# Kernel tuning notes

Hardware: AMD Instinct MI355X
Metric: run time of the kernel (lower is better)

The kernel has to match this reference:

```python
import jax, jax.numpy as jnp
import numpy as np

CAP = 15.0
EPS = 1e-6
NUM_HEADS = 16
HEAD_DIM = 64

def _rmsnorm(x, w):
    xf = x.astype(jnp.float32)
    var = jnp.mean(xf * xf, axis=-1, keepdims=True)
    return w * (xf * jax.lax.rsqrt(var + EPS)).astype(x.dtype)

def _gate(g):
    # sigmoid(soft_cap(g)) with cap 15
    return jax.nn.sigmoid(CAP * jnp.tanh(g / CAP))

def setup_inputs() -> dict:
    key = jax.random.key(0)
    ks = jax.random.split(key, 4)
    B, S, D = 4, 2048, 1024
    H, Dh = NUM_HEADS, HEAD_DIM
    return {
        "x": jax.random.normal(ks[0], (B, S, D), jnp.float32),
        "hidden_state": jnp.zeros((B, H, Dh, Dh), jnp.float32),
        "w_rms": jnp.ones((D,), jnp.float32),
        "w_qkv": jax.random.normal(ks[1], (D, 3 * H * Dh), jnp.float32) * 0.02,
        "w_gate": jax.random.normal(ks[2], (D, 3 * H), jnp.float32) * 0.02,
        "w_out": jax.random.normal(ks[3], (D, D), jnp.float32) * 0.02,
    }

def reference(x, hidden_state, w_rms, w_qkv, w_gate, w_out):
    B, S, D = x.shape
    H, Dh = NUM_HEADS, HEAD_DIM
    residual = x
    xn = _rmsnorm(x, w_rms)
    qkv = (xn @ w_qkv).reshape(B, S, 3, H, Dh)
    q, k, v = qkv[:, :, 0], qkv[:, :, 1], qkv[:, :, 2]  # [B,S,H,Dh]
    gates = _gate((xn @ w_gate).reshape(B, S, 3, H))
    i_g, f_g, o_g = gates[:, :, 0], gates[:, :, 1], gates[:, :, 2]  # [B,S,H]

    # time-major for scan: [S,B,H,...]
    def tm(a):
        return jnp.moveaxis(a, 1, 0)

    def step(state, inp):
        qt, kt, vt, it, ft, ot = inp  # [B,H,Dh]/[B,H]
        kv = kt[..., :, None] * vt[..., None, :]            # [B,H,Dh,Dh]
        state = ft[..., None, None] * state + it[..., None, None] * kv
        h = jnp.einsum('bhd,bhde->bhe', qt, state) * ot[..., None]
        return state, h

    _, h_seq = jax.lax.scan(step, hidden_state,
                            (tm(q), tm(k), tm(v), tm(i_g), tm(f_g), tm(o_g)))
    out = jnp.moveaxis(h_seq, 0, 1).reshape(B, S, H * Dh) @ w_out
    return residual + out
```

## Files before the change

kernel.cpp:

```cpp
#include <hip/hip_runtime.h>
#include <math.h>

typedef unsigned short u16;
typedef unsigned int   u32;
typedef __bf16 bf16x8 __attribute__((ext_vector_type(8)));
typedef float  f32x4  __attribute__((ext_vector_type(4)));

#define NBATCH 4
#define SEQ    2048
#define DIM    1024
#define NH     16
#define BH     64
#define NC     32
#define ROWS   8192
#define N1     3328

__device__ __forceinline__ u16 f2bf(float f) {
  u32 u = __builtin_bit_cast(u32, f);
  u32 r = u + 0x7fffu + ((u >> 16) & 1u);
  return (u16)(r >> 16);
}
__device__ __forceinline__ float bf2f(u16 h) {
  return __builtin_bit_cast(float, (u32)h << 16);
}

__device__ __forceinline__ void gl2lds16(const u16* g, u16* l) {
  __builtin_amdgcn_global_load_lds(
      (const __attribute__((address_space(1))) u32*)g,
      (__attribute__((address_space(3))) u32*)l, 16, 0, 0);
}

__global__ __launch_bounds__(256) void prep_all(const float* __restrict__ x,
                                                const float* __restrict__ w_rms,
                                                u16* __restrict__ xn,
                                                const float* __restrict__ Wqkv,
                                                const float* __restrict__ Wout,
                                                const float* __restrict__ wg,
                                                u16* __restrict__ BtQkv, u16* __restrict__ BtOut) {
  __shared__ float tile[32][33];
  __shared__ float red[4];
  const int bid = blockIdx.x;
  if (bid < 8192) {
    const int row = bid, tid = threadIdx.x;
    const float4 xv = *(const float4*)&x[(size_t)row * 1024 + tid * 4];
    float ss = xv.x * xv.x + xv.y * xv.y + xv.z * xv.z + xv.w * xv.w;
    #pragma unroll
    for (int off = 32; off > 0; off >>= 1) ss += __shfl_down(ss, off);
    if ((tid & 63) == 0) red[tid >> 6] = ss;
    __syncthreads();
    const float tot = red[0] + red[1] + red[2] + red[3];
    const float scale = rsqrtf(tot * (1.0f / 1024.0f) + 1e-6f);
    const float4 wv = *(const float4*)&w_rms[tid * 4];
    const u16 o0 = f2bf(xv.x * scale * wv.x), o1 = f2bf(xv.y * scale * wv.y);
    const u16 o2 = f2bf(xv.z * scale * wv.z), o3 = f2bf(xv.w * scale * wv.w);
    uint2 ov;
    ov.x = (u32)o0 | ((u32)o1 << 16);
    ov.y = (u32)o2 | ((u32)o3 << 16);
    *(uint2*)&xn[(size_t)row * 1024 + tid * 4] = ov;
  } else {
    const int pb = bid - 8192;
    const int bx = pb % 129, by = pb / 129;
    const int tx = threadIdx.x & 31, ty = threadIdx.x >> 5;
    if (bx < 128) {
      const float* W; u16* Bt; int N, n0;
      if (bx < 96) { W = Wqkv; Bt = BtQkv; N = 3072; n0 = bx * 32; }
      else         { W = Wout; Bt = BtOut; N = 1024; n0 = (bx - 96) * 32; }
      const int k0 = by * 32;
      #pragma unroll
      for (int i = 0; i < 4; i++)
        tile[ty + i * 8][tx] = W[(size_t)(k0 + ty + i * 8) * N + n0 + tx];
      __syncthreads();
      #pragma unroll
      for (int i = 0; i < 4; i++)
        Bt[(size_t)(n0 + ty + i * 8) * 1024 + k0 + tx] = f2bf(tile[tx][ty + i * 8]);
    } else {
      const int tid = threadIdx.x;
      #pragma unroll
      for (int gg = 0; gg < 8; gg++) {
        const int g = by * 8 + gg;
        #pragma unroll
        for (int kk = 0; kk < 4; kk++) {
          const int k = kk * 256 + tid;
          u16 v = 0;
          if (g < 48) v = f2bf(wg[(size_t)k * 48 + g]);
          BtQkv[(size_t)(3072 + g) * 1024 + k] = v;
        }
      }
    }
  }
}


#define FENCE asm volatile("" ::: "memory")
#define SBAR  do { FENCE; __builtin_amdgcn_s_barrier(); FENCE; } while (0)
#define WAITV4 do { FENCE; asm volatile("s_waitcnt vmcnt(4)" ::: "memory"); } while (0)
#define WAITV2 do { FENCE; asm volatile("s_waitcnt vmcnt(2)" ::: "memory"); } while (0)
#define WAITV0 do { FENCE; asm volatile("s_waitcnt vmcnt(0)" ::: "memory"); } while (0)

#define STAGE_A(BUF, HALF, TILE) do { \
  const u16* s_ = Abase + (size_t)(TILE) * 64 + (size_t)(HALF) * 131072; \
  u16* l_ = &lds[((BUF) * 4 + (HALF)) * 8192 + tid * 8]; \
  gl2lds16(s_, l_); gl2lds16(s_ + 65536, l_ + 4096); \
} while (0)

#define STAGE_B(BUF, HALF, TILE) do { \
  const u16* s_ = Bbase + (size_t)(TILE) * 64 + (size_t)(HALF) * 131072; \
  u16* l_ = &lds[((BUF) * 4 + 2 + (HALF)) * 8192 + tid * 8]; \
  gl2lds16(s_, l_); gl2lds16(s_ + 65536, l_ + 4096); \
} while (0)

#define READ_A(ALDS, MH) do { \
  _Pragma("unroll") \
  for (int mi_ = 0; mi_ < 4; ++mi_) { \
    af[mi_][0] = *(const bf16x8*)((ALDS) + (MH) * 4096 + mi_ * 1024 + co0); \
    af[mi_][1] = *(const bf16x8*)((ALDS) + (MH) * 4096 + mi_ * 1024 + co1); \
  } \
} while (0)

#define READ_B(BLDS, NH) do { \
  _Pragma("unroll") \
  for (int ni_ = 0; ni_ < 2; ++ni_) { \
    bfr[NH][ni_][0] = *(const bf16x8*)((BLDS) + (NH) * 2048 + ni_ * 1024 + co0); \
    bfr[NH][ni_][1] = *(const bf16x8*)((BLDS) + (NH) * 2048 + ni_ * 1024 + co1); \
  } \
} while (0)

#define MFMA16(MH, NH) do { \
  __builtin_amdgcn_s_setprio(1); \
  _Pragma("unroll") \
  for (int mi_ = 0; mi_ < 4; ++mi_) { \
    _Pragma("unroll") \
    for (int ni_ = 0; ni_ < 2; ++ni_) { \
      acc[(MH)*4+mi_][(NH)*2+ni_] = __builtin_amdgcn_mfma_f32_16x16x32_bf16( \
          af[mi_][0], bfr[NH][ni_][0], acc[(MH)*4+mi_][(NH)*2+ni_], 0, 0, 0); \
      acc[(MH)*4+mi_][(NH)*2+ni_] = __builtin_amdgcn_mfma_f32_16x16x32_bf16( \
          af[mi_][1], bfr[NH][ni_][1], acc[(MH)*4+mi_][(NH)*2+ni_], 0, 0, 0); \
    } \
  } \
  __builtin_amdgcn_s_setprio(0); \
} while (0)

#define GITER4(T, FULL) do { \
   \
  STAGE_A(1, 0, 2*(T)+1); STAGE_A(1, 1, 2*(T)+1); \
  READ_A(aLds0, 0); READ_B(bLds0, 0); READ_B(bLds0, 1); \
  SBAR; MFMA16(0, 0); MFMA16(0, 1); SBAR; \
   \
  if (FULL) { STAGE_B(0, 0, 2*(T)+2); STAGE_B(0, 1, 2*(T)+2); } \
  READ_A(aLds0, 1); \
  SBAR; MFMA16(1, 0); MFMA16(1, 1); if (FULL) { WAITV4; } else { WAITV0; } SBAR; \
   \
  if (FULL) { STAGE_A(0, 0, 2*(T)+2); STAGE_A(0, 1, 2*(T)+2); } \
  READ_A(aLds1, 0); READ_B(bLds1, 0); READ_B(bLds1, 1); \
  SBAR; MFMA16(0, 0); MFMA16(0, 1); SBAR; \
   \
  if (FULL) { STAGE_B(1, 0, 2*(T)+3); STAGE_B(1, 1, 2*(T)+3); } \
  READ_A(aLds1, 1); \
  SBAR; MFMA16(1, 0); MFMA16(1, 1); if (FULL) { WAITV4; } SBAR; \
} while (0)

#define CORE_SETUP(AROWBASE, BCOLBASE) \
  const int tid = threadIdx.x; \
  const int lane = tid & 63, wave = tid >> 6; \
  const int q = lane >> 4, m16 = lane & 15; \
  const int wm = wave & 1, wn = wave >> 1; \
  const int sx = m16 & 7; \
  const int co0 = (q ^ sx) * 8; \
  const int co1 = ((4 + q) ^ sx) * 8; \
  const int r0 = tid >> 3, pc = tid & 7; \
  const int lcg = pc ^ (r0 & 7); \
  const u16* Abase = (AROWBASE) + (size_t)r0 * 1024 + lcg * 8; \
  const u16* Bbase = (BCOLBASE) + (size_t)r0 * 1024 + lcg * 8; \
  const u16* aLds0 = &lds[wm * 8192 + m16 * 64]; \
  const u16* aLds1 = aLds0 + 32768; \
  const u16* bLds0 = &lds[16384 + (wn >> 1) * 8192 + ((wn & 1) * 64 + m16) * 64]; \
  const u16* bLds1 = bLds0 + 32768; \
  bf16x8 af[4][2]; \
  bf16x8 bfr[2][2][2]; \
  f32x4 acc[8][4] = {};

#define CORE_RUN16() do { \
  STAGE_A(0, 0, 0); STAGE_A(0, 1, 0); STAGE_B(0, 0, 0); STAGE_B(0, 1, 0); \
  STAGE_B(1, 0, 1); STAGE_B(1, 1, 1); \
  WAITV4; SBAR; \
  _Pragma("unroll 1") \
  for (int t = 0; t < 7; ++t) GITER4(t, 1); \
  GITER4(7, 0); \
} while (0)

__global__ __launch_bounds__(512, 2) void gemm_qkv(const u16* __restrict__ A, const u16* __restrict__ Bt,
                                                   u16* __restrict__ Qb, u16* __restrict__ Kb,
                                                   u16* __restrict__ Vb, float* __restrict__ gates) {
  __shared__ __attribute__((aligned(16))) u16 lds[65536];

  const int g = blockIdx.x;
  const int swz = (g & 7) * 52 + (g >> 3);
  const int bm = swz & 31, bn = swz >> 5;
  const int rowBase = bm * 256, colBase = bn * 256;

  CORE_SETUP(A + (size_t)rowBase * 1024, Bt + (size_t)colBase * 1024);
  CORE_RUN16();

  const int rr = lane >> 2, co = (lane & 3) * 16;
  if (colBase < 3072) {
    const int which = colBase >> 10;
    u16* dstBase = (which == 0) ? Qb : ((which == 1) ? Kb : Vb);
    const int b = rowBase >> 11;
    const int h = ((colBase & 1023) >> 6) + wn;
    const int tRow0 = (rowBase & 2047) + wm * 128;
    u16* headBase = dstBase + ((size_t)(b * 16 + h)) * 2048 * 64;
    u16* scratch = lds + wave * 1024;
    #pragma unroll
    for (int mi = 0; mi < 8; ++mi) {
      #pragma unroll
      for (int bj = 0; bj < 4; ++bj)
        #pragma unroll
        for (int r = 0; r < 4; ++r)
          scratch[(q * 4 + r) * 64 + bj * 16 + m16] = f2bf(acc[mi][bj][r]);
      const uint4 d0 = *(const uint4*)&scratch[rr * 64 + co];
      const uint4 d1 = *(const uint4*)&scratch[rr * 64 + co + 8];
      u16* gp = headBase + (size_t)(tRow0 + mi * 16 + rr) * 64 + co;
      *(uint4*)gp = d0;
      *(uint4*)(gp + 8) = d1;
    }
  } else {
    if (wn == 0) {
      #pragma unroll
      for (int ai = 0; ai < 8; ++ai)
        #pragma unroll
        for (int bj = 0; bj < 3; ++bj)
          #pragma unroll
          for (int r = 0; r < 4; ++r) {
            const int grow = rowBase + wm * 128 + ai * 16 + q * 4 + r;
            const int b = grow >> 11, tt = grow & 2047;
            const float v = acc[ai][bj][r];
            const float gg = 1.0f / (1.0f + __expf(-(15.0f * tanhf(v * (1.0f / 15.0f)))));
            gates[((size_t)bj * 64 + (b * 16 + m16)) * 2048 + tt] = gg;
          }
    }
  }
}


#define STAGE_AO(BUF, TILE) do { \
  const u16* s_ = Abase + (size_t)(TILE) * 64; \
  u16* l_ = &lds[(BUF) * 24576 + tid * 8]; \
  gl2lds16(s_, l_); gl2lds16(s_ + 65536, l_ + 4096); \
} while (0)

#define STAGE_BO(BUF, HALF, TILE) do { \
  const u16* s_ = Bbase + (size_t)(TILE) * 64 + (size_t)(HALF) * 131072; \
  u16* l_ = &lds[(BUF) * 24576 + 8192 + (HALF) * 8192 + tid * 8]; \
  gl2lds16(s_, l_); gl2lds16(s_ + 65536, l_ + 4096); \
} while (0)

#define READ_AO(ALDS) do { \
  _Pragma("unroll") \
  for (int mi_ = 0; mi_ < 4; ++mi_) { \
    af[mi_][0] = *(const bf16x8*)((ALDS) + mi_ * 1024 + co0); \
    af[mi_][1] = *(const bf16x8*)((ALDS) + mi_ * 1024 + co1); \
  } \
} while (0)

#define MFMA16O(NH) do { \
  __builtin_amdgcn_s_setprio(1); \
  _Pragma("unroll") \
  for (int mi_ = 0; mi_ < 4; ++mi_) { \
    _Pragma("unroll") \
    for (int ni_ = 0; ni_ < 2; ++ni_) { \
      acc[mi_][(NH)*2+ni_] = __builtin_amdgcn_mfma_f32_16x16x32_bf16( \
          af[mi_][0], bfr[NH][ni_][0], acc[mi_][(NH)*2+ni_], 0, 0, 0); \
      acc[mi_][(NH)*2+ni_] = __builtin_amdgcn_mfma_f32_16x16x32_bf16( \
          af[mi_][1], bfr[NH][ni_][1], acc[mi_][(NH)*2+ni_], 0, 0, 0); \
    } \
  } \
  __builtin_amdgcn_s_setprio(0); \
} while (0)

#define GITER_O(T, FULL) do { \
   STAGE_BO(1, 0, 2*(T)+1); STAGE_BO(1, 1, 2*(T)+1); \
         READ_AO(aLds0); READ_B(bLds0, 0); \
         SBAR; MFMA16O(0); SBAR; \
   if (FULL) STAGE_AO(0, 2*(T)+2); \
         READ_B(bLds0, 1); \
         SBAR; MFMA16O(1); if (FULL) { WAITV2; } else { WAITV0; } SBAR; \
   if (FULL) { STAGE_BO(0, 0, 2*(T)+2); STAGE_BO(0, 1, 2*(T)+2); } \
         READ_AO(aLds1); READ_B(bLds1, 0); \
         SBAR; MFMA16O(0); SBAR; \
   if (FULL) STAGE_AO(1, 2*(T)+3); \
         READ_B(bLds1, 1); \
         SBAR; MFMA16O(1); if (FULL) { WAITV2; } SBAR; \
} while (0)

__global__ __launch_bounds__(512, 2) void gemm_out(const u16* __restrict__ A, const u16* __restrict__ Bt,
                                                   const float* __restrict__ resid,
                                                   float* __restrict__ out) {
  __shared__ __attribute__((aligned(16))) u16 lds[49152];

  const int g = blockIdx.x;
  const int swz = (g & 7) * 32 + (g >> 3);
  const int bm = swz & 63, bn = swz >> 6;
  const int rowBase = bm * 128, colBase = bn * 256;

  const int tid = threadIdx.x;
  const int lane = tid & 63, wave = tid >> 6;
  const int q = lane >> 4, m16 = lane & 15;
  const int wm = wave & 1, wn = wave >> 1;
  const int sx = m16 & 7;
  const int co0 = (q ^ sx) * 8;
  const int co1 = ((4 + q) ^ sx) * 8;
  const int r0 = tid >> 3, pc = tid & 7;
  const int lcg = pc ^ (r0 & 7);
  const u16* Abase = A  + (size_t)rowBase * 1024 + (size_t)r0 * 1024 + lcg * 8;
  const u16* Bbase = Bt + (size_t)colBase * 1024 + (size_t)r0 * 1024 + lcg * 8;
  const u16* aLds0 = &lds[wm * 4096 + m16 * 64];
  const u16* aLds1 = aLds0 + 24576;
  const u16* bLds0 = &lds[8192 + (wn >> 1) * 8192 + ((wn & 1) * 64 + m16) * 64];
  const u16* bLds1 = bLds0 + 24576;
  bf16x8 af[4][2];
  bf16x8 bfr[2][2][2];
  f32x4 acc[4][4] = {};

  STAGE_AO(0, 0); STAGE_BO(0, 0, 0); STAGE_BO(0, 1, 0);
  STAGE_AO(1, 1);
  WAITV2; SBAR;

  #pragma unroll 1
  for (int t = 0; t < 7; ++t) GITER_O(t, 1);
  GITER_O(7, 0);

  const int colW = colBase + wn * 64;
  #pragma unroll
  for (int mi = 0; mi < 4; ++mi)
    #pragma unroll
    for (int bj = 0; bj < 4; ++bj)
      #pragma unroll
      for (int r = 0; r < 4; ++r) {
        const int grow = rowBase + wm * 64 + mi * 16 + q * 4 + r;
        const int gcol = colW + bj * 16 + m16;
        const size_t idx = (size_t)grow * 1024 + gcol;
        out[idx] = acc[mi][bj][r] + resid[idx];
      }
}

__global__ __launch_bounds__(256) void passA_k(const u16* __restrict__ Qb, const u16* __restrict__ Kb,
                                               const u16* __restrict__ Vb,
                                               const float* __restrict__ gates,
                                               float* __restrict__ la,
                                               u16* __restrict__ Mbuf, u16* __restrict__ hseq) {
  __shared__ u16 Ql[64][72], Kl[64][72], KTl[64][72], VTl[64][72], Pl[64][72];
  __shared__ float laS[64], iS[64];
  const int tid = threadIdx.x;
  const int bh = blockIdx.x >> 5, c = blockIdx.x & 31;
  const int lane = tid & 63, w = tid >> 6;
  const int q = lane >> 4, m16 = lane & 15;
  const size_t base = ((size_t)bh * 2048 + c * 64) * 64;
  const int toff = c * 64;

  if (tid < 64) {
    float lg = __logf(gates[(size_t)(64 + bh) * 2048 + toff + tid]);
    #pragma unroll
    for (int off = 1; off < 64; off <<= 1) {
      const float y = __shfl_up(lg, off);
      if (tid >= off) lg += y;
    }
    laS[tid] = lg;
    iS[tid] = gates[(size_t)bh * 2048 + toff + tid];
    la[(size_t)bh * 2048 + toff + tid] = lg;
  }
  __syncthreads();

  {
    const int s = tid >> 2, db = (tid & 3) * 16;
    const float wk = __expf(laS[63] - laS[s]) * iS[s];
    const uint4 q0 = *(const uint4*)&Qb[base + s * 64 + db];
    const uint4 q1 = *(const uint4*)&Qb[base + s * 64 + db + 8];
    *(uint4*)&Ql[s][db] = q0;
    *(uint4*)&Ql[s][db + 8] = q1;
    const uint4 k0 = *(const uint4*)&Kb[base + s * 64 + db];
    const uint4 k1 = *(const uint4*)&Kb[base + s * 64 + db + 8];
    *(uint4*)&Kl[s][db] = k0;
    *(uint4*)&Kl[s][db + 8] = k1;
    u16 ktmp[16];
    *(uint4*)&ktmp[0] = k0;
    *(uint4*)&ktmp[8] = k1;
    const uint4 v0 = *(const uint4*)&Vb[base + s * 64 + db];
    const uint4 v1 = *(const uint4*)&Vb[base + s * 64 + db + 8];
    u16 vtmp[16];
    *(uint4*)&vtmp[0] = v0;
    *(uint4*)&vtmp[8] = v1;
    const int rot = s + (db >> 4);
    #pragma unroll
    for (int j = 0; j < 16; j++) {
      const int jj = (j + rot) & 15;
      KTl[db + jj][s] = f2bf(wk * bf2f(ktmp[jj]));
      VTl[db + jj][s] = vtmp[jj];
    }
  }
  __syncthreads();

  f32x4 pacc[4] = {};
  #pragma unroll
  for (int ks = 0; ks < 2; ks++) {
    const bf16x8 aq = *(const bf16x8*)&Ql[w * 16 + m16][ks * 32 + q * 8];
    #pragma unroll
    for (int ni = 0; ni < 4; ni++) {
      const bf16x8 bk = *(const bf16x8*)&Kl[ni * 16 + m16][ks * 32 + q * 8];
      pacc[ni] = __builtin_amdgcn_mfma_f32_16x16x32_bf16(aq, bk, pacc[ni], 0, 0, 0);
    }
  }
  #pragma unroll
  for (int ni = 0; ni < 4; ni++)
    #pragma unroll
    for (int r = 0; r < 4; r++) {
      const int tt = w * 16 + q * 4 + r, ss = ni * 16 + m16;
      float Wts = 0.0f;
      if (ss <= tt) Wts = __expf(laS[tt] - laS[ss]) * iS[ss];
      Pl[tt][ss] = f2bf(pacc[ni][r] * Wts);
    }
  __syncthreads();

  f32x4 hacc[4] = {}, macc[4] = {};
  #pragma unroll
  for (int ks = 0; ks < 2; ks++) {
    const bf16x8 ap = *(const bf16x8*)&Pl[w * 16 + m16][ks * 32 + q * 8];
    const bf16x8 av = *(const bf16x8*)&VTl[w * 16 + m16][ks * 32 + q * 8];
    #pragma unroll
    for (int ni = 0; ni < 4; ni++) {
      const bf16x8 bv = *(const bf16x8*)&VTl[ni * 16 + m16][ks * 32 + q * 8];
      const bf16x8 bk = *(const bf16x8*)&KTl[ni * 16 + m16][ks * 32 + q * 8];
      hacc[ni] = __builtin_amdgcn_mfma_f32_16x16x32_bf16(ap, bv, hacc[ni], 0, 0, 0);
      macc[ni] = __builtin_amdgcn_mfma_f32_16x16x32_bf16(av, bk, macc[ni], 0, 0, 0);
    }
  }

  __syncthreads();
  #pragma unroll
  for (int ni = 0; ni < 4; ni++)
    #pragma unroll
    for (int r = 0; r < 4; r++) {
      const int tt = w * 16 + q * 4 + r, e = ni * 16 + m16;
      Pl[tt][e] = f2bf(hacc[ni][r]);
      Kl[tt][e] = f2bf(macc[ni][r]);
    }
  __syncthreads();
  {
    const int s = tid >> 2, db = (tid & 3) * 16;
    const int b = bh >> 4, h = bh & 15;
    u16* hp = &hseq[((size_t)b * 2048 + c * 64 + s) * 1024 + h * 64 + db];
    *(uint4*)hp       = *(const uint4*)&Pl[s][db];
    *(uint4*)(hp + 8) = *(const uint4*)&Pl[s][db + 8];
    u16* mp = &Mbuf[(((size_t)bh * 32 + c) * 64 + s) * 64 + db];
    *(uint4*)mp       = *(const uint4*)&Kl[s][db];
    *(uint4*)(mp + 8) = *(const uint4*)&Kl[s][db + 8];
  }
}

__global__ __launch_bounds__(256) void passB_k(u16* __restrict__ Mbuf,
                                               const float* __restrict__ hidden,
                                               const float* __restrict__ la) {
  const int bh = blockIdx.x >> 4;
  const int e = (blockIdx.x & 15) * 256 + threadIdx.x;
  __shared__ float Gs[32];
  if (threadIdx.x < 32)
    Gs[threadIdx.x] = __expf(la[(size_t)bh * 2048 + threadIdx.x * 64 + 63]);
  __syncthreads();
  const int eRow = e >> 6, dCol = e & 63;
  float st = hidden[(size_t)bh * 4096 + dCol * 64 + eRow];
  u16* M = &Mbuf[(size_t)bh * 32 * 4096 + e];
  float m0 = bf2f(M[0]);
  float m1 = bf2f(M[4096]);
  #pragma unroll 4
  for (int c = 0; c < 32; c++) {
    const float m_cur = m0;
    m0 = m1;
    if (c < 30) m1 = bf2f(M[(size_t)(c + 2) * 4096]);
    M[(size_t)c * 4096] = f2bf(st);
    st = Gs[c] * st + m_cur;
  }
}

__global__ __launch_bounds__(256) void passC_k(const u16* __restrict__ Qb,
                                               const u16* __restrict__ SprevT,
                                               const float* __restrict__ la,
                                               const float* __restrict__ gates,
                                               u16* __restrict__ hseq) {
  __shared__ u16 aQl[64][72], STl[64][72];
  __shared__ float hstage[64][68];
  __shared__ float laS[64], oS[64];
  const int tid = threadIdx.x;
  const int bh = blockIdx.x >> 5, c = blockIdx.x & 31;
  const int lane = tid & 63, w = tid >> 6;
  const int q = lane >> 4, m16 = lane & 15;
  const size_t base = ((size_t)bh * 2048 + c * 64) * 64;
  const int toff = c * 64;
  if (tid < 64) {
    laS[tid] = la[(size_t)bh * 2048 + toff + tid];
    oS[tid] = gates[(size_t)(128 + bh) * 2048 + toff + tid];
  }
  {
    const int s = tid >> 2, db = (tid & 3) * 16;
    *(uint4*)&aQl[s][db]     = *(const uint4*)&Qb[base + s * 64 + db];
    *(uint4*)&aQl[s][db + 8] = *(const uint4*)&Qb[base + s * 64 + db + 8];
    const u16* SpT = &SprevT[((size_t)bh * 32 + c) * 4096];
    *(uint4*)&STl[s][db]     = *(const uint4*)&SpT[s * 64 + db];
    *(uint4*)&STl[s][db + 8] = *(const uint4*)&SpT[s * 64 + db + 8];
  }
  __syncthreads();
  f32x4 acc[4] = {};
  #pragma unroll
  for (int ks = 0; ks < 2; ks++) {
    const bf16x8 a = *(const bf16x8*)&aQl[w * 16 + m16][ks * 32 + q * 8];
    #pragma unroll
    for (int ni = 0; ni < 4; ni++) {
      const bf16x8 bb = *(const bf16x8*)&STl[ni * 16 + m16][ks * 32 + q * 8];
      acc[ni] = __builtin_amdgcn_mfma_f32_16x16x32_bf16(a, bb, acc[ni], 0, 0, 0);
    }
  }
  #pragma unroll
  for (int ni = 0; ni < 4; ni++)
    #pragma unroll
    for (int r = 0; r < 4; r++)
      hstage[w * 16 + q * 4 + r][ni * 16 + m16] = acc[ni][r];
  __syncthreads();
  {
    const int s = tid >> 2, db = (tid & 3) * 16;
    const int b = bh >> 4, h = bh & 15;
    const float a_t = __expf(laS[s]);
    const float o = oS[s];
    u16* hp = &hseq[((size_t)b * 2048 + c * 64 + s) * 1024 + h * 64 + db];
    uint4 h0 = *(const uint4*)hp, h1 = *(const uint4*)(hp + 8);
    u16 hv[16];
    *(uint4*)&hv[0] = h0;
    *(uint4*)&hv[8] = h1;
    float sv[16];
    *(float4*)&sv[0]  = *(const float4*)&hstage[s][db];
    *(float4*)&sv[4]  = *(const float4*)&hstage[s][db + 4];
    *(float4*)&sv[8]  = *(const float4*)&hstage[s][db + 8];
    *(float4*)&sv[12] = *(const float4*)&hstage[s][db + 12];
    u16 ov[16];
    #pragma unroll
    for (int j = 0; j < 16; j++)
      ov[j] = f2bf(o * (bf2f(hv[j]) + a_t * sv[j]));
    *(uint4*)hp       = *(const uint4*)&ov[0];
    *(uint4*)(hp + 8) = *(const uint4*)&ov[8];
  }
}

extern "C" void kernel_launch(void* const* d_in, const int* in_sizes, int n_in,
                              void* d_out, int out_size, void* d_ws, size_t ws_size,
                              hipStream_t stream) {
  (void)in_sizes; (void)n_in; (void)out_size; (void)ws_size;
  const float* x      = (const float*)d_in[0];
  const float* hidden = (const float*)d_in[1];
  const float* w_rms  = (const float*)d_in[2];
  const float* w_qkv  = (const float*)d_in[3];
  const float* w_gate = (const float*)d_in[4];
  const float* w_out  = (const float*)d_in[5];
  float* out = (float*)d_out;

  char* p = (char*)d_ws;
  u16* wqkvT = (u16*)p;  p += (size_t)N1 * 1024 * 2;
  u16* woutT = (u16*)p;  p += (size_t)1024 * 1024 * 2;
  u16* xn    = (u16*)p;  p += (size_t)ROWS * 1024 * 2;
  u16* Qb    = (u16*)p;  p += (size_t)BH * 2048 * 64 * 2;
  u16* Kb    = (u16*)p;  p += (size_t)BH * 2048 * 64 * 2;
  u16* Vb    = (u16*)p;  p += (size_t)BH * 2048 * 64 * 2;
  float* gates = (float*)p; p += (size_t)3 * BH * 2048 * 4;
  float* la    = (float*)p; p += (size_t)BH * 2048 * 4;
  u16* Mbuf  = (u16*)p;  p += (size_t)BH * NC * 4096 * 2;
  u16* hseq  = (u16*)p;  p += (size_t)ROWS * 1024 * 2;

  prep_all<<<12320, 256, 0, stream>>>(x, w_rms, xn, w_qkv, w_out, w_gate, wqkvT, woutT);
  gemm_qkv<<<416, 512, 0, stream>>>(xn, wqkvT, Qb, Kb, Vb, gates);
  passA_k<<<BH * NC, 256, 0, stream>>>(Qb, Kb, Vb, gates, la, Mbuf, hseq);
  passB_k<<<BH * 16, 256, 0, stream>>>(Mbuf, hidden, la);
  passC_k<<<BH * NC, 256, 0, stream>>>(Qb, Mbuf, la, gates, hseq);
  gemm_out<<<256, 512, 0, stream>>>(hseq, woutT, x, out);
}
```

Baseline: 243.3 us.

## Retile QKV GEMM to 128x256 tiles with K=32 steps and higher occupancy

The QKV projection GEMM changes from 256x256 block tiles with K-steps of 64 and 128KB of LDS to 128x256 tiles with K-steps of 32, a 48KB LDS double buffer and a simpler one-barrier-pair pipeline. The grid doubles to 832 blocks and launch bounds target 4 blocks per CU. The aim is more resident waves and better load balance across CUs. In exchange each block reuses less data, so global and LDS traffic per FLOP rises, and the pipeline takes more iterations with more barriers.

```diff
diff --git a/kernel.cpp b/kernel.cpp
--- a/kernel.cpp
+++ b/kernel.cpp
@@ -90,157 +90,140 @@
   }
 }
 
-
 #define FENCE asm volatile("" ::: "memory")
 #define SBAR  do { FENCE; __builtin_amdgcn_s_barrier(); FENCE; } while (0)
-#define WAITV4 do { FENCE; asm volatile("s_waitcnt vmcnt(4)" ::: "memory"); } while (0)
+#define LGKM0 do { FENCE; asm volatile("s_waitcnt lgkmcnt(0)" ::: "memory"); } while (0)
+#define WAITV3 do { FENCE; asm volatile("s_waitcnt vmcnt(3)" ::: "memory"); } while (0)
 #define WAITV2 do { FENCE; asm volatile("s_waitcnt vmcnt(2)" ::: "memory"); } while (0)
 #define WAITV0 do { FENCE; asm volatile("s_waitcnt vmcnt(0)" ::: "memory"); } while (0)
 
-#define STAGE_A(BUF, HALF, TILE) do { \
-  const u16* s_ = Abase + (size_t)(TILE) * 64 + (size_t)(HALF) * 131072; \
-  u16* l_ = &lds[((BUF) * 4 + (HALF)) * 8192 + tid * 8]; \
-  gl2lds16(s_, l_); gl2lds16(s_ + 65536, l_ + 4096); \
-} while (0)
-
-#define STAGE_B(BUF, HALF, TILE) do { \
-  const u16* s_ = Bbase + (size_t)(TILE) * 64 + (size_t)(HALF) * 131072; \
-  u16* l_ = &lds[((BUF) * 4 + 2 + (HALF)) * 8192 + tid * 8]; \
-  gl2lds16(s_, l_); gl2lds16(s_ + 65536, l_ + 4096); \
-} while (0)
-
-#define READ_A(ALDS, MH) do { \
+
+#define QSTA(BUF, TILE) do { \
+  gl2lds16(gA + (size_t)(TILE) * 32, &lds[(BUF) * 12288 + tid * 8]); \
+} while (0)
+
+#define QSTB(BUF, TILE) do { \
+  const u16* s_ = gB + (size_t)(TILE) * 32; \
+  u16* l_ = &lds[(BUF) * 12288 + 4096 + tid * 8]; \
+  gl2lds16(s_, l_); gl2lds16(s_ + 131072, l_ + 4096); \
+} while (0)
+
+#define QREAD(BUF) do { \
   _Pragma("unroll") \
-  for (int mi_ = 0; mi_ < 4; ++mi_) { \
-    af[mi_][0] = *(const bf16x8*)((ALDS) + (MH) * 4096 + mi_ * 1024 + co0); \
-    af[mi_][1] = *(const bf16x8*)((ALDS) + (MH) * 4096 + mi_ * 1024 + co1); \
-  } \
-} while (0)
-
-#define READ_B(BLDS, NH) do { \
+  for (int mi_ = 0; mi_ < 4; ++mi_) \
+    af[mi_] = *(const bf16x8*)(aL + (BUF) * 12288 + mi_ * 512); \
   _Pragma("unroll") \
-  for (int ni_ = 0; ni_ < 2; ++ni_) { \
-    bfr[NH][ni_][0] = *(const bf16x8*)((BLDS) + (NH) * 2048 + ni_ * 1024 + co0); \
-    bfr[NH][ni_][1] = *(const bf16x8*)((BLDS) + (NH) * 2048 + ni_ * 1024 + co1); \
-  } \
-} while (0)
-
-#define MFMA16(MH, NH) do { \
+  for (int ni_ = 0; ni_ < 4; ++ni_) \
+    bfr[ni_] = *(const bf16x8*)(bL + (BUF) * 12288 + ni_ * 512); \
+} while (0)
+
+#define QMFMA do { \
   __builtin_amdgcn_s_setprio(1); \
   _Pragma("unroll") \
-  for (int mi_ = 0; mi_ < 4; ++mi_) { \
+  for (int mi_ = 0; mi_ < 4; ++mi_) \
     _Pragma("unroll") \
-    for (int ni_ = 0; ni_ < 2; ++ni_) { \
-      acc[(MH)*4+mi_][(NH)*2+ni_] = __builtin_amdgcn_mfma_f32_16x16x32_bf16( \
-          af[mi_][0], bfr[NH][ni_][0], acc[(MH)*4+mi_][(NH)*2+ni_], 0, 0, 0); \
-      acc[(MH)*4+mi_][(NH)*2+ni_] = __builtin_amdgcn_mfma_f32_16x16x32_bf16( \
-          af[mi_][1], bfr[NH][ni_][1], acc[(MH)*4+mi_][(NH)*2+ni_], 0, 0, 0); \
-    } \
-  } \
+    for (int ni_ = 0; ni_ < 4; ++ni_) \
+      acc[mi_][ni_] = __builtin_amdgcn_mfma_f32_16x16x32_bf16( \
+          af[mi_], bfr[ni_], acc[mi_][ni_], 0, 0, 0); \
   __builtin_amdgcn_s_setprio(0); \
 } while (0)
 
-#define GITER4(T, FULL) do { \
-   \
-  STAGE_A(1, 0, 2*(T)+1); STAGE_A(1, 1, 2*(T)+1); \
-  READ_A(aLds0, 0); READ_B(bLds0, 0); READ_B(bLds0, 1); \
-  SBAR; MFMA16(0, 0); MFMA16(0, 1); SBAR; \
-   \
-  if (FULL) { STAGE_B(0, 0, 2*(T)+2); STAGE_B(0, 1, 2*(T)+2); } \
-  READ_A(aLds0, 1); \
-  SBAR; MFMA16(1, 0); MFMA16(1, 1); if (FULL) { WAITV4; } else { WAITV0; } SBAR; \
-   \
-  if (FULL) { STAGE_A(0, 0, 2*(T)+2); STAGE_A(0, 1, 2*(T)+2); } \
-  READ_A(aLds1, 0); READ_B(bLds1, 0); READ_B(bLds1, 1); \
-  SBAR; MFMA16(0, 0); MFMA16(0, 1); SBAR; \
-   \
-  if (FULL) { STAGE_B(1, 0, 2*(T)+3); STAGE_B(1, 1, 2*(T)+3); } \
-  READ_A(aLds1, 1); \
-  SBAR; MFMA16(1, 0); MFMA16(1, 1); if (FULL) { WAITV4; } SBAR; \
-} while (0)
-
-#define CORE_SETUP(AROWBASE, BCOLBASE) \
-  const int tid = threadIdx.x; \
-  const int lane = tid & 63, wave = tid >> 6; \
-  const int q = lane >> 4, m16 = lane & 15; \
-  const int wm = wave & 1, wn = wave >> 1; \
-  const int sx = m16 & 7; \
-  const int co0 = (q ^ sx) * 8; \
-  const int co1 = ((4 + q) ^ sx) * 8; \
-  const int r0 = tid >> 3, pc = tid & 7; \
-  const int lcg = pc ^ (r0 & 7); \
-  const u16* Abase = (AROWBASE) + (size_t)r0 * 1024 + lcg * 8; \
-  const u16* Bbase = (BCOLBASE) + (size_t)r0 * 1024 + lcg * 8; \
-  const u16* aLds0 = &lds[wm * 8192 + m16 * 64]; \
-  const u16* aLds1 = aLds0 + 32768; \
-  const u16* bLds0 = &lds[16384 + (wn >> 1) * 8192 + ((wn & 1) * 64 + m16) * 64]; \
-  const u16* bLds1 = bLds0 + 32768; \
-  bf16x8 af[4][2]; \
-  bf16x8 bfr[2][2][2]; \
-  f32x4 acc[8][4] = {};
-
-#define CORE_RUN16() do { \
-  STAGE_A(0, 0, 0); STAGE_A(0, 1, 0); STAGE_B(0, 0, 0); STAGE_B(0, 1, 0); \
-  STAGE_B(1, 0, 1); STAGE_B(1, 1, 1); \
-  WAITV4; SBAR; \
-  _Pragma("unroll 1") \
-  for (int t = 0; t < 7; ++t) GITER4(t, 1); \
-  GITER4(7, 0); \
-} while (0)
-
-__global__ __launch_bounds__(512, 2) void gemm_qkv(const u16* __restrict__ A, const u16* __restrict__ Bt,
+#define QSTEP(CUR, KB, FULL) do { \
+  QREAD(CUR); \
+  LGKM0; SBAR; \
+  if (FULL) { QSTA(CUR, (KB) + 2); QSTB(CUR, (KB) + 2); } \
+  QMFMA; \
+  if (FULL) { WAITV3; } else if ((KB) == 30) { WAITV0; } \
+  SBAR; \
+} while (0)
+
+__global__ __launch_bounds__(512, 4) void gemm_qkv(const u16* __restrict__ A, const u16* __restrict__ Bt,
                                                    u16* __restrict__ Qb, u16* __restrict__ Kb,
                                                    u16* __restrict__ Vb, float* __restrict__ gates) {
-  __shared__ __attribute__((aligned(16))) u16 lds[65536];
+  __shared__ __attribute__((aligned(16))) u16 lds[24576];
 
   const int g = blockIdx.x;
-  const int swz = (g & 7) * 52 + (g >> 3);
-  const int bm = swz & 31, bn = swz >> 5;
-  const int rowBase = bm * 256, colBase = bn * 256;
-
-  CORE_SETUP(A + (size_t)rowBase * 1024, Bt + (size_t)colBase * 1024);
-  CORE_RUN16();
-
-  const int rr = lane >> 2, co = (lane & 3) * 16;
+  const int swz = (g & 7) * 104 + (g >> 3);
+  const int bm = swz & 63, bn = swz >> 6;
+  const int rowBase = bm * 128, colBase = bn * 256;
+
+  const int tid = threadIdx.x;
+  const int lane = tid & 63, wave = tid >> 6;
+  const int q = lane >> 4, m16 = lane & 15;
+  const int wm = wave & 1, wn = wave >> 1;
+  const int co = (q ^ ((m16 >> 1) & 3)) * 8;
+  const u16* aL = &lds[wm * 2048 + m16 * 32 + co];
+  const u16* bL = &lds[4096 + wn * 2048 + m16 * 32 + co];
+
+  const int r0 = tid >> 2, pc = tid & 3;
+  const int lcg = pc ^ ((tid >> 3) & 3);
+  const u16* gA = A  + (size_t)(rowBase + r0) * 1024 + lcg * 8;
+  const u16* gB = Bt + (size_t)(colBase + r0) * 1024 + lcg * 8;
+
+  bf16x8 af[4];
+  bf16x8 bfr[4];
+  f32x4 acc[4][4] = {};
+
+  QSTA(0, 0); QSTB(0, 0);
+  QSTA(1, 1); QSTB(1, 1);
+  WAITV3; SBAR;
+
+  #pragma unroll 1
+  for (int t7 = 0; t7 < 15; ++t7) {
+    QSTEP(0, 2 * t7,     1);
+    QSTEP(1, 2 * t7 + 1, 1);
+  }
+  QSTEP(0, 30, 0);
+  QSTEP(1, 31, 0);
+
+  const int rr = lane >> 2, co2 = (lane & 3) * 16;
   if (colBase < 3072) {
     const int which = colBase >> 10;
     u16* dstBase = (which == 0) ? Qb : ((which == 1) ? Kb : Vb);
     const int b = rowBase >> 11;
     const int h = ((colBase & 1023) >> 6) + wn;
-    const int tRow0 = (rowBase & 2047) + wm * 128;
+    const int tRow0 = (rowBase & 2047) + wm * 64;
     u16* headBase = dstBase + ((size_t)(b * 16 + h)) * 2048 * 64;
     u16* scratch = lds + wave * 1024;
     #pragma unroll
-    for (int mi = 0; mi < 8; ++mi) {
+    for (int mi = 0; mi < 4; ++mi) {
       #pragma unroll
-      for (int bj = 0; bj < 4; ++bj)
+      for (int ni = 0; ni < 4; ++ni)
         #pragma unroll
         for (int r = 0; r < 4; ++r)
-          scratch[(q * 4 + r) * 64 + bj * 16 + m16] = f2bf(acc[mi][bj][r]);
-      const uint4 d0 = *(const uint4*)&scratch[rr * 64 + co];
-      const uint4 d1 = *(const uint4*)&scratch[rr * 64 + co + 8];
-      u16* gp = headBase + (size_t)(tRow0 + mi * 16 + rr) * 64 + co;
+          scratch[(q * 4 + r) * 64 + ni * 16 + m16] = f2bf(acc[mi][ni][r]);
+      const uint4 d0 = *(const uint4*)&scratch[rr * 64 + co2];
+      const uint4 d1 = *(const uint4*)&scratch[rr * 64 + co2 + 8];
+      u16* gp = headBase + (size_t)(tRow0 + mi * 16 + rr) * 64 + co2;
       *(uint4*)gp = d0;
       *(uint4*)(gp + 8) = d1;
     }
   } else {
     if (wn == 0) {
       #pragma unroll
-      for (int ai = 0; ai < 8; ++ai)
+      for (int mi = 0; mi < 4; ++mi)
         #pragma unroll
-        for (int bj = 0; bj < 3; ++bj)
+        for (int ni = 0; ni < 3; ++ni)
           #pragma unroll
           for (int r = 0; r < 4; ++r) {
-            const int grow = rowBase + wm * 128 + ai * 16 + q * 4 + r;
+            const int grow = rowBase + wm * 64 + mi * 16 + q * 4 + r;
             const int b = grow >> 11, tt = grow & 2047;
-            const float v = acc[ai][bj][r];
+            const float v = acc[mi][ni][r];
             const float gg = 1.0f / (1.0f + __expf(-(15.0f * tanhf(v * (1.0f / 15.0f)))));
-            gates[((size_t)bj * 64 + (b * 16 + m16)) * 2048 + tt] = gg;
+            gates[((size_t)ni * 64 + (b * 16 + m16)) * 2048 + tt] = gg;
           }
     }
   }
 }
 
+
+#define READ_B(BLDS, NH) do { \
+  _Pragma("unroll") \
+  for (int ni_ = 0; ni_ < 2; ++ni_) { \
+    bfrO[NH][ni_][0] = *(const bf16x8*)((BLDS) + (NH) * 2048 + ni_ * 1024 + co0); \
+    bfrO[NH][ni_][1] = *(const bf16x8*)((BLDS) + (NH) * 2048 + ni_ * 1024 + co1); \
+  } \
+} while (0)
 
 #define STAGE_AO(BUF, TILE) do { \
   const u16* s_ = Abase + (size_t)(TILE) * 64; \
@@ -257,8 +240,8 @@
 #define READ_AO(ALDS) do { \
   _Pragma("unroll") \
   for (int mi_ = 0; mi_ < 4; ++mi_) { \
-    af[mi_][0] = *(const bf16x8*)((ALDS) + mi_ * 1024 + co0); \
-    af[mi_][1] = *(const bf16x8*)((ALDS) + mi_ * 1024 + co1); \
+    afO[mi_][0] = *(const bf16x8*)((ALDS) + mi_ * 1024 + co0); \
+    afO[mi_][1] = *(const bf16x8*)((ALDS) + mi_ * 1024 + co1); \
   } \
 } while (0)
 
@@ -269,9 +252,9 @@
     _Pragma("unroll") \
     for (int ni_ = 0; ni_ < 2; ++ni_) { \
       acc[mi_][(NH)*2+ni_] = __builtin_amdgcn_mfma_f32_16x16x32_bf16( \
-          af[mi_][0], bfr[NH][ni_][0], acc[mi_][(NH)*2+ni_], 0, 0, 0); \
+          afO[mi_][0], bfrO[NH][ni_][0], acc[mi_][(NH)*2+ni_], 0, 0, 0); \
       acc[mi_][(NH)*2+ni_] = __builtin_amdgcn_mfma_f32_16x16x32_bf16( \
-          af[mi_][1], bfr[NH][ni_][1], acc[mi_][(NH)*2+ni_], 0, 0, 0); \
+          afO[mi_][1], bfrO[NH][ni_][1], acc[mi_][(NH)*2+ni_], 0, 0, 0); \
     } \
   } \
   __builtin_amdgcn_s_setprio(0); \
@@ -317,8 +300,8 @@
   const u16* aLds1 = aLds0 + 24576;
   const u16* bLds0 = &lds[8192 + (wn >> 1) * 8192 + ((wn & 1) * 64 + m16) * 64];
   const u16* bLds1 = bLds0 + 24576;
-  bf16x8 af[4][2];
-  bf16x8 bfr[2][2][2];
+  bf16x8 afO[4][2];
+  bf16x8 bfrO[2][2][2];
   f32x4 acc[4][4] = {};
 
   STAGE_AO(0, 0); STAGE_BO(0, 0, 0); STAGE_BO(0, 1, 0);
@@ -572,7 +555,7 @@
   u16* hseq  = (u16*)p;  p += (size_t)ROWS * 1024 * 2;
 
   prep_all<<<12320, 256, 0, stream>>>(x, w_rms, xn, w_qkv, w_out, w_gate, wqkvT, woutT);
-  gemm_qkv<<<416, 512, 0, stream>>>(xn, wqkvT, Qb, Kb, Vb, gates);
+  gemm_qkv<<<832, 512, 0, stream>>>(xn, wqkvT, Qb, Kb, Vb, gates);
   passA_k<<<BH * NC, 256, 0, stream>>>(Qb, Kb, Vb, gates, la, Mbuf, hseq);
   passB_k<<<BH * 16, 256, 0, stream>>>(Mbuf, hidden, la);
   passC_k<<<BH * NC, 256, 0, stream>>>(Qb, Mbuf, la, gates, hseq);
```

Measured after the change: 251.0 us. +3.2%, slower.
